# Kernel tuning notes

Hardware: AMD Instinct MI355X
Metric: run time of the kernel (lower is better)

## Reference

```python
import jax, jax.numpy as jnp
import numpy as np
from jax import lax

V, E, H, T, S = 100000, 256, 512, 9, 4096
HH = H // 2
START, STOP = 7, 8
NEG = -10000.0


def setup_inputs() -> dict:
    key = jax.random.key(0)
    ks = jax.random.split(key, 16)
    def n(k, shape, scale=0.1):
        return jax.random.normal(k, shape, jnp.float32) * scale
    sentence = jax.random.randint(ks[0], (S,), 0, V)
    embed = n(ks[1], (V, E), 1.0)
    w_ih_f = n(ks[2], (4 * HH, E)); w_hh_f = n(ks[3], (4 * HH, HH))
    b_ih_f = n(ks[4], (4 * HH,));   b_hh_f = n(ks[5], (4 * HH,))
    w_ih_b = n(ks[6], (4 * HH, E)); w_hh_b = n(ks[7], (4 * HH, HH))
    b_ih_b = n(ks[8], (4 * HH,));   b_hh_b = n(ks[9], (4 * HH,))
    h0 = n(ks[10], (2, HH), 1.0)  # init_hidden: randn (2,1,HH), batch squeezed
    c0 = n(ks[11], (2, HH), 1.0)
    W_out = n(ks[12], (T, H)); b_out = n(ks[13], (T,))
    transitions = jax.random.normal(ks[14], (T, T), jnp.float32)
    transitions = transitions.at[START, :].set(NEG).at[:, STOP].set(NEG)
    return dict(sentence=sentence, embed=embed,
                w_ih_f=w_ih_f, w_hh_f=w_hh_f, b_ih_f=b_ih_f, b_hh_f=b_hh_f,
                w_ih_b=w_ih_b, w_hh_b=w_hh_b, b_ih_b=b_ih_b, b_hh_b=b_hh_b,
                h0=h0, c0=c0, W_out=W_out, b_out=b_out, transitions=transitions)


def _lstm_dir(x_gates, h0, c0, w_hh):
    # x_gates: [S, 4*HH] = x @ w_ih.T + b_ih + b_hh (precomputed input part)
    def step(carry, xg):
        h, c = carry
        g = xg + h @ w_hh.T
        i, f, gg, o = jnp.split(g, 4)  # torch gate order: i, f, g, o
        i = jax.nn.sigmoid(i); f = jax.nn.sigmoid(f)
        gg = jnp.tanh(gg);     o = jax.nn.sigmoid(o)
        c = f * c + i * gg
        h = o * jnp.tanh(c)
        return (h, c), h
    _, hs = lax.scan(step, (h0, c0), x_gates)
    return hs  # [S, HH]


def reference(sentence, embed, w_ih_f, w_hh_f, b_ih_f, b_hh_f,
              w_ih_b, w_hh_b, b_ih_b, b_hh_b, h0, c0, W_out, b_out, transitions):
    x = embed[sentence]  # [S, E]
    # bidirectional LSTM, batch=1
    hf = _lstm_dir(x @ w_ih_f.T + b_ih_f + b_hh_f, h0[0], c0[0], w_hh_f)
    hb = _lstm_dir((x @ w_ih_b.T + b_ih_b + b_hh_b)[::-1], h0[1], c0[1], w_hh_b)[::-1]
    lstm_out = jnp.concatenate([hf, hb], axis=-1)          # [S, H]
    frames = lstm_out @ W_out.T + b_out                     # [S, T] emission scores

    # Viterbi-style decode (faithful: alpha updated by logsumexp, backpointers by argmax)
    alpha0 = jnp.full((T,), NEG, jnp.float32).at[START].set(0.0)
    def vstep(alpha, frame):
        smat = alpha[:, None] + frame[None, :] + transitions  # [T, T]
        bp = jnp.argmax(smat, axis=0)
        return jax.nn.logsumexp(smat, axis=0), bp
    alpha, bps = lax.scan(vstep, alpha0, frames)            # bps: [S, T]

    final = alpha + transitions[:, STOP]                     # [T]
    best = jnp.argmax(final)
    score = jax.nn.logsumexp(final)

    # backtrack over bps[1:] in reverse
    def bstep(tag, bp):
        nt = bp[tag]
        return nt, nt
    _, path_rev = lax.scan(bstep, best, bps[1:][::-1])
    tag_seq = jnp.concatenate([path_rev[::-1], best[None]])  # [S]
    return score, tag_seq
```

## Files before the change

kernel.cpp:

```cpp
#include <hip/hip_runtime.h>
#include <hip/hip_bf16.h>

#define SEQ   4096
#define EMB   256
#define HHID  256
#define G4    1024
#define NT    9
#define TSTART 7
#define TSTOP  8
#define NEGV  (-10000.0f)
#define POISON 0xAAAAAAAAu

#define WS_XG_F   0u
#define WS_XG_B   16777216u
#define WS_HF     33554432u
#define WS_HB     37748736u
#define WS_FRAMES 41943040u
#define WS_BPS    42090496u
#define WS_MISC   42127360u

__global__ __launch_bounds__(256) void xgate_kernel(
    const int* __restrict__ sentence, const float* __restrict__ embed,
    const float* __restrict__ w_ih_f, const float* __restrict__ b_ih_f,
    const float* __restrict__ b_hh_f,
    const float* __restrict__ w_ih_b, const float* __restrict__ b_ih_b,
    const float* __restrict__ b_hh_b,
    float* __restrict__ xg_f, float* __restrict__ xg_b)
{
    const int st  = blockIdx.x;
    const int dir = blockIdx.y;
    const float* w  = dir ? w_ih_b : w_ih_f;
    const float* bi = dir ? b_ih_b : b_ih_f;
    const float* bh = dir ? b_hh_b : b_hh_f;
    float* xg = dir ? xg_b : xg_f;
    const int t = threadIdx.x;

    __shared__ float x_t[EMB][16];
    for (int sl = 0; sl < 16; ++sl) {
        int s   = st * 16 + sl;
        int tok = sentence[s];
        x_t[t][sl] = embed[(size_t)tok * EMB + t];
    }
    __syncthreads();

    float acc[4][16];
    #pragma unroll
    for (int q = 0; q < 4; ++q)
        #pragma unroll
        for (int sl = 0; sl < 16; ++sl) acc[q][sl] = 0.f;

    #pragma unroll 4
    for (int e = 0; e < EMB; ++e) {
        float w0 = w[(size_t)(t        ) * EMB + e];
        float w1 = w[(size_t)(t + 256  ) * EMB + e];
        float w2 = w[(size_t)(t + 512  ) * EMB + e];
        float w3 = w[(size_t)(t + 768  ) * EMB + e];
        #pragma unroll
        for (int sl = 0; sl < 16; ++sl) {
            float xv = x_t[e][sl];
            acc[0][sl] += w0 * xv;
            acc[1][sl] += w1 * xv;
            acc[2][sl] += w2 * xv;
            acc[3][sl] += w3 * xv;
        }
    }

    #pragma unroll
    for (int q = 0; q < 4; ++q) {
        int g = t + 256 * q;
        float bb = bi[g] + bh[g];
        for (int sl = 0; sl < 16; ++sl) {
            xg[(size_t)(st * 16 + sl) * G4 + g] = acc[q][sl] + bb;
        }
    }
}

__global__ __launch_bounds__(256, 1) void lstm_kernel(
    const float* __restrict__ xg_f, const float* __restrict__ xg_b,
    const float* __restrict__ w_hh_f, const float* __restrict__ w_hh_b,
    const float* __restrict__ h0, const float* __restrict__ c0,
    float* __restrict__ hf, float* __restrict__ hb)
{
    const int bx    = blockIdx.x;
    const int dir   = bx >> 3;
    const int slice = bx & 7;
    const int t     = threadIdx.x;

    const float* xg   = dir ? xg_b  : xg_f;
    const float* w_hh = dir ? w_hh_b : w_hh_f;
    float* hout = dir ? hb : hf;

    __shared__ float h_lds[HHID];
    __shared__ float gbuf[128];

    const int lr   = t >> 1;
    const int half = t & 1;
    const int type = lr >> 5;
    const int ul   = lr & 31;
    const int unit = slice * 32 + ul;
    const int grow = type * HHID + unit;

    float w[128];
    #pragma unroll
    for (int j = 0; j < 128; ++j)
        w[j] = w_hh[(size_t)grow * HHID + half * 128 + j];

    float c_reg = 0.f;
    if (t < 32) c_reg = c0[dir * HHID + slice * 32 + t];

    for (int n = 0; n < SEQ; ++n) {
        const int s = dir ? (SEQ - 1 - n) : n;

        float xgi = 0.f, xgff = 0.f, xgg = 0.f, xgo = 0.f;
        if (t < 32) {
            const float* xb = xg + (size_t)s * G4 + slice * 32 + t;
            xgi  = xb[0];
            xgff = xb[256];
            xgg  = xb[512];
            xgo  = xb[768];
        }

        if (n == 0) {
            h_lds[t] = h0[dir * HHID + t];
        } else if (t < 64) {
            const int sp = dir ? (s + 1) : (s - 1);
            unsigned int* src = (unsigned int*)(hout + (size_t)sp * HHID) + t * 4;
            unsigned got = 0;
            float hv[4];
            while (got != 0xFu) {
                #pragma unroll
                for (int j = 0; j < 4; ++j) {
                    if (!((got >> j) & 1u)) {
                        unsigned v = __hip_atomic_load(src + j, __ATOMIC_RELAXED,
                                                       __HIP_MEMORY_SCOPE_AGENT);
                        if (v != POISON) {
                            hv[j] = __uint_as_float(v);
                            got |= 1u << j;
                        }
                    }
                }
            }
            #pragma unroll
            for (int j = 0; j < 4; ++j) h_lds[t * 4 + j] = hv[j];
        }
        __syncthreads();

        float acc = 0.f;
        const float4* hv4 = (const float4*)(h_lds + half * 128);
        #pragma unroll
        for (int j4 = 0; j4 < 32; ++j4) {
            float4 hv = hv4[j4];
            acc += w[j4 * 4 + 0] * hv.x;
            acc += w[j4 * 4 + 1] * hv.y;
            acc += w[j4 * 4 + 2] * hv.z;
            acc += w[j4 * 4 + 3] * hv.w;
        }
        acc += __shfl_xor(acc, 1);
        if (half == 0) gbuf[lr] = acc;
        __syncthreads();

        if (t < 32) {
            float gi = gbuf[t]      + xgi;
            float gf = gbuf[32 + t] + xgff;
            float gg = gbuf[64 + t] + xgg;
            float go = gbuf[96 + t] + xgo;
            float iv = 1.f / (1.f + __expf(-gi));
            float fv = 1.f / (1.f + __expf(-gf));
            float gv = 1.f - 2.f / (__expf(2.f * gg) + 1.f);
            float ov = 1.f / (1.f + __expf(-go));
            float c  = fv * c_reg + iv * gv;
            c_reg = c;
            float h  = ov * (1.f - 2.f / (__expf(2.f * c) + 1.f));
            unsigned int* dst = (unsigned int*)(hout + (size_t)s * HHID) + slice * 32 + t;
            __hip_atomic_store(dst, __float_as_uint(h), __ATOMIC_RELAXED,
                               __HIP_MEMORY_SCOPE_AGENT);
        }
    }
}

__global__ __launch_bounds__(256) void frames_kernel(
    const float* __restrict__ hf, const float* __restrict__ hb,
    const float* __restrict__ W_out, const float* __restrict__ b_out,
    float* __restrict__ frames)
{
    int o = blockIdx.x * 256 + threadIdx.x;
    if (o >= SEQ * NT) return;
    int s = o / NT;
    int j = o - s * NT;
    const float4* a0 = (const float4*)(hf + (size_t)s * HHID);
    const float4* a1 = (const float4*)(hb + (size_t)s * HHID);
    const float4* w0 = (const float4*)(W_out + (size_t)j * 512);
    const float4* w1 = w0 + 64;
    float acc = 0.f;
    #pragma unroll 8
    for (int i = 0; i < 64; ++i) {
        float4 a = a0[i], b = w0[i];
        acc += a.x * b.x + a.y * b.y + a.z * b.z + a.w * b.w;
        float4 c = a1[i], d = w1[i];
        acc += c.x * d.x + c.y * d.y + c.z * d.z + c.w * d.w;
    }
    frames[o] = acc + b_out[j];
}

__global__ __launch_bounds__(64) void crf_kernel(
    const float* __restrict__ frames, const float* __restrict__ trans,
    unsigned char* __restrict__ bps, float* __restrict__ dout,
    int* __restrict__ misc)
{
    __shared__ float fr[512 * NT];
    __shared__ float alpha[16];
    const int t = threadIdx.x;

    float trow[NT];
    if (t < NT) {
        #pragma unroll
        for (int i = 0; i < NT; ++i) trow[i] = trans[i * NT + t];
        alpha[t] = (t == TSTART) ? 0.f : NEGV;
    }

    for (int chunk = 0; chunk < 8; ++chunk) {
        __syncthreads();
        for (int idx = t; idx < 512 * NT; idx += 64)
            fr[idx] = frames[chunk * 512 * NT + idx];
        __syncthreads();

        for (int sl = 0; sl < 512; ++sl) {
            const int s = chunk * 512 + sl;
            float anew = 0.f;
            int   am   = 0;
            if (t < NT) {
                float v[NT];
                #pragma unroll
                for (int i = 0; i < NT; ++i) v[i] = alpha[i] + trow[i];
                float mx = v[0];
                #pragma unroll
                for (int i = 1; i < NT; ++i)
                    if (v[i] > mx) { mx = v[i]; am = i; }
                float sum = 0.f;
                #pragma unroll
                for (int i = 0; i < NT; ++i) sum += __expf(v[i] - mx);
                anew = fr[sl * NT + t] + mx + __logf(sum);
            }
            __syncthreads();
            if (t < NT) {
                alpha[t] = anew;
                bps[(size_t)s * NT + t] = (unsigned char)am;
            }
            __syncthreads();
        }
    }

    if (t == 0) {
        float fin[NT];
        #pragma unroll
        for (int j = 0; j < NT; ++j) fin[j] = alpha[j] + trans[j * NT + TSTOP];
        float mx = fin[0];
        int best = 0;
        #pragma unroll
        for (int j = 1; j < NT; ++j)
            if (fin[j] > mx) { mx = fin[j]; best = j; }
        float sum = 0.f;
        #pragma unroll
        for (int j = 0; j < NT; ++j) sum += __expf(fin[j] - mx);
        dout[0] = mx + __logf(sum);
        misc[0] = best;
    }
}

__global__ __launch_bounds__(256) void backtrack_kernel(
    const unsigned char* __restrict__ bps, const int* __restrict__ misc,
    float* __restrict__ dout)
{
    __shared__ unsigned char bl[SEQ * NT];
    __shared__ unsigned char tags[SEQ];
    const int t = threadIdx.x;

    const unsigned int* src = (const unsigned int*)bps;
    unsigned int* dst = (unsigned int*)bl;
    for (int i = t; i < SEQ * NT / 4; i += 256) dst[i] = src[i];
    __syncthreads();

    if (t == 0) {
        int cur = misc[0];
        tags[SEQ - 1] = (unsigned char)cur;
        for (int s = SEQ - 2; s >= 0; --s) {
            cur = bl[(s + 1) * NT + cur];
            tags[s] = (unsigned char)cur;
        }
    }
    __syncthreads();
    for (int i = t; i < SEQ; i += 256)
        dout[1 + i] = (float)tags[i];
}

extern "C" void kernel_launch(void* const* d_in, const int* in_sizes, int n_in,
                              void* d_out, int out_size, void* d_ws, size_t ws_size,
                              hipStream_t stream)
{
    const int*   sentence = (const int*)  d_in[0];
    const float* embed    = (const float*)d_in[1];
    const float* w_ih_f   = (const float*)d_in[2];
    const float* w_hh_f   = (const float*)d_in[3];
    const float* b_ih_f   = (const float*)d_in[4];
    const float* b_hh_f   = (const float*)d_in[5];
    const float* w_ih_b   = (const float*)d_in[6];
    const float* w_hh_b   = (const float*)d_in[7];
    const float* b_ih_b   = (const float*)d_in[8];
    const float* b_hh_b   = (const float*)d_in[9];
    const float* h0       = (const float*)d_in[10];
    const float* c0       = (const float*)d_in[11];
    const float* W_out    = (const float*)d_in[12];
    const float* b_out    = (const float*)d_in[13];
    const float* trans    = (const float*)d_in[14];

    float* out = (float*)d_out;
    char*  ws  = (char*)d_ws;

    float* xg_f   = (float*)(ws + WS_XG_F);
    float* xg_b   = (float*)(ws + WS_XG_B);
    float* hf     = (float*)(ws + WS_HF);
    float* hb     = (float*)(ws + WS_HB);
    float* frames = (float*)(ws + WS_FRAMES);
    unsigned char* bps = (unsigned char*)(ws + WS_BPS);
    int* misc = (int*)(ws + WS_MISC);

    hipMemsetAsync(hf, 0xAA, 2u * SEQ * HHID * sizeof(float), stream);

    xgate_kernel<<<dim3(256, 2), 256, 0, stream>>>(
        sentence, embed, w_ih_f, b_ih_f, b_hh_f, w_ih_b, b_ih_b, b_hh_b,
        xg_f, xg_b);

    lstm_kernel<<<16, 256, 0, stream>>>(
        xg_f, xg_b, w_hh_f, w_hh_b, h0, c0, hf, hb);

    frames_kernel<<<(SEQ * NT + 255) / 256, 256, 0, stream>>>(
        hf, hb, W_out, b_out, frames);

    crf_kernel<<<1, 64, 0, stream>>>(frames, trans, bps, out, misc);

    backtrack_kernel<<<1, 256, 0, stream>>>(bps, misc, out);
}
```

Measured before the change: 10.00 ms.

## Keep CRF alpha in registers via shuffles and fuse backtrack into CRF kernel

The CRF recursion now holds alpha in a register per lane and broadcasts it with wave shuffles, which removes the two __syncthreads per timestep. Backpointers stay in LDS and the backtrack runs inside the same kernel, so the global bps round trip and one kernel launch go away. An empty asm barrier is also added on the LSTM weight registers to pin them in VGPRs. The backtrack is still a serial single-thread loop, now writing each tag straight to global memory instead of staging through LDS.

Result: no change. 10.20 ms (+2.0%).

```diff
diff --git a/kernel.cpp b/kernel.cpp
--- a/kernel.cpp
+++ b/kernel.cpp
@@ -16,8 +16,6 @@
 #define WS_HF     33554432u
 #define WS_HB     37748736u
 #define WS_FRAMES 41943040u
-#define WS_BPS    42090496u
-#define WS_MISC   42127360u
 
 __global__ __launch_bounds__(256) void xgate_kernel(
     const int* __restrict__ sentence, const float* __restrict__ embed,
@@ -104,6 +102,9 @@
     #pragma unroll
     for (int j = 0; j < 128; ++j)
         w[j] = w_hh[(size_t)grow * HHID + half * 128 + j];
+    #pragma unroll
+    for (int j = 0; j < 128; ++j)
+        asm volatile("" : "+v"(w[j]));
 
     float c_reg = 0.f;
     if (t < 32) c_reg = c0[dir * HHID + slice * 32 + t];
@@ -204,93 +205,74 @@
 
 __global__ __launch_bounds__(64) void crf_kernel(
     const float* __restrict__ frames, const float* __restrict__ trans,
-    unsigned char* __restrict__ bps, float* __restrict__ dout,
-    int* __restrict__ misc)
+    float* __restrict__ dout)
 {
     __shared__ float fr[512 * NT];
-    __shared__ float alpha[16];
+    __shared__ unsigned char bpl[SEQ * NT];
     const int t = threadIdx.x;
+    const int tc = (t < NT) ? t : 0;
 
     float trow[NT];
+    #pragma unroll
+    for (int i = 0; i < NT; ++i) trow[i] = 0.f;
     if (t < NT) {
         #pragma unroll
         for (int i = 0; i < NT; ++i) trow[i] = trans[i * NT + t];
-        alpha[t] = (t == TSTART) ? 0.f : NEGV;
-    }
+    }
+    float alpha = (t == TSTART) ? 0.f : NEGV;
 
     for (int chunk = 0; chunk < 8; ++chunk) {
-        __syncthreads();
         for (int idx = t; idx < 512 * NT; idx += 64)
             fr[idx] = frames[chunk * 512 * NT + idx];
         __syncthreads();
 
         for (int sl = 0; sl < 512; ++sl) {
             const int s = chunk * 512 + sl;
-            float anew = 0.f;
-            int   am   = 0;
+            float v[NT];
+            #pragma unroll
+            for (int i = 0; i < NT; ++i)
+                v[i] = __shfl(alpha, i) + trow[i];
+            float mx = v[0];
+            int   am = 0;
+            #pragma unroll
+            for (int i = 1; i < NT; ++i)
+                if (v[i] > mx) { mx = v[i]; am = i; }
+            float sum = 0.f;
+            #pragma unroll
+            for (int i = 0; i < NT; ++i) sum += __expf(v[i] - mx);
+            float anew = fr[sl * NT + tc] + mx + __logf(sum);
             if (t < NT) {
-                float v[NT];
-                #pragma unroll
-                for (int i = 0; i < NT; ++i) v[i] = alpha[i] + trow[i];
-                float mx = v[0];
-                #pragma unroll
-                for (int i = 1; i < NT; ++i)
-                    if (v[i] > mx) { mx = v[i]; am = i; }
-                float sum = 0.f;
-                #pragma unroll
-                for (int i = 0; i < NT; ++i) sum += __expf(v[i] - mx);
-                anew = fr[sl * NT + t] + mx + __logf(sum);
+                bpl[s * NT + t] = (unsigned char)am;
+                alpha = anew;
             }
-            __syncthreads();
-            if (t < NT) {
-                alpha[t] = anew;
-                bps[(size_t)s * NT + t] = (unsigned char)am;
-            }
-            __syncthreads();
-        }
-    }
+        }
+        __syncthreads();
+    }
+
+    float fin = NEGV;
+    if (t < NT) fin = alpha + trans[t * NT + TSTOP];
+    float f[NT];
+    #pragma unroll
+    for (int j = 0; j < NT; ++j) f[j] = __shfl(fin, j);
 
     if (t == 0) {
-        float fin[NT];
-        #pragma unroll
-        for (int j = 0; j < NT; ++j) fin[j] = alpha[j] + trans[j * NT + TSTOP];
-        float mx = fin[0];
+        float mx = f[0];
         int best = 0;
         #pragma unroll
         for (int j = 1; j < NT; ++j)
-            if (fin[j] > mx) { mx = fin[j]; best = j; }
+            if (f[j] > mx) { mx = f[j]; best = j; }
         float sum = 0.f;
         #pragma unroll
-        for (int j = 0; j < NT; ++j) sum += __expf(fin[j] - mx);
+        for (int j = 0; j < NT; ++j) sum += __expf(f[j] - mx);
         dout[0] = mx + __logf(sum);
-        misc[0] = best;
-    }
-}
-
-__global__ __launch_bounds__(256) void backtrack_kernel(
-    const unsigned char* __restrict__ bps, const int* __restrict__ misc,
-    float* __restrict__ dout)
-{
-    __shared__ unsigned char bl[SEQ * NT];
-    __shared__ unsigned char tags[SEQ];
-    const int t = threadIdx.x;
-
-    const unsigned int* src = (const unsigned int*)bps;
-    unsigned int* dst = (unsigned int*)bl;
-    for (int i = t; i < SEQ * NT / 4; i += 256) dst[i] = src[i];
-    __syncthreads();
-
-    if (t == 0) {
-        int cur = misc[0];
-        tags[SEQ - 1] = (unsigned char)cur;
+
+        int cur = best;
+        dout[1 + SEQ - 1] = (float)cur;
         for (int s = SEQ - 2; s >= 0; --s) {
-            cur = bl[(s + 1) * NT + cur];
-            tags[s] = (unsigned char)cur;
-        }
-    }
-    __syncthreads();
-    for (int i = t; i < SEQ; i += 256)
-        dout[1 + i] = (float)tags[i];
+            cur = bpl[(s + 1) * NT + cur];
+            dout[1 + s] = (float)cur;
+        }
+    }
 }
 
 extern "C" void kernel_launch(void* const* d_in, const int* in_sizes, int n_in,
@@ -321,8 +303,6 @@
     float* hf     = (float*)(ws + WS_HF);
     float* hb     = (float*)(ws + WS_HB);
     float* frames = (float*)(ws + WS_FRAMES);
-    unsigned char* bps = (unsigned char*)(ws + WS_BPS);
-    int* misc = (int*)(ws + WS_MISC);
 
     hipMemsetAsync(hf, 0xAA, 2u * SEQ * HHID * sizeof(float), stream);
 
@@ -336,7 +316,5 @@
     frames_kernel<<<(SEQ * NT + 255) / 256, 256, 0, stream>>>(
         hf, hb, W_out, b_out, frames);
 
-    crf_kernel<<<1, 64, 0, stream>>>(frames, trans, bps, out, misc);
-
-    backtrack_kernel<<<1, 256, 0, stream>>>(bps, misc, out);
-}
+    crf_kernel<<<1, 64, 0, stream>>>(frames, trans, out);
+}
```
